# Optimization experiments

Measured on AMD Instinct MI355X. Metric: run time of the kernel, lower is better.

The kernel has to match this reference:

```python
import jax, jax.numpy as jnp
import numpy as np

B, N, D, P_IN, P_OUT = 8, 2048, 32, 8, 4


def setup_inputs() -> dict:
    key = jax.random.key(0)
    k1, k2, k3, k4 = jax.random.split(key, 4)
    U = jax.random.normal(k1, (B, N, D, P_IN), dtype=jnp.float32)
    A = jax.random.uniform(k2, (B, N, N), dtype=jnp.float32)
    W_self = jax.random.normal(k3, (P_IN, P_OUT), dtype=jnp.float32) * 0.01
    W_neigh = jax.random.normal(k4, (P_IN, P_OUT), dtype=jnp.float32) * 0.01
    bias = jnp.zeros((1, 1, 1, P_OUT), dtype=jnp.float32)
    return {"U": U, "A": A, "W_self": W_self, "W_neigh": W_neigh, "bias": bias}


def _stiefel_projection(Y_flat):
    # Polar factor: Y = W S V^T  ->  proj = W V^T (same as Y @ (Y^T Y)^{-1/2})
    u, _, vt = jnp.linalg.svd(Y_flat, full_matrices=False)
    return u @ vt


def reference(U, A, W_self, W_neigh, bias):
    # U: (B,N,d,p_in); A: (B,N,N)
    M_self = jnp.einsum('bndi,io->bndo', U, W_self)
    M_neigh = jnp.einsum('bndi,io->bndo', U, W_neigh)
    # dense neighborhood aggregation: A @ reshape(M_neigh, (B,N,d*p_out))
    M_agg = jnp.einsum('bnm,bmdo->bndo', A, M_neigh)
    Y = jax.nn.relu(M_self + M_agg + bias)
    Y_flat = Y.reshape(B * N, D, P_OUT)
    U_proj = _stiefel_projection(Y_flat)
    return U_proj.reshape(B, N, D, P_OUT)
```

## Files before the change

kernel.cpp:

```cpp
#include <hip/hip_runtime.h>
#include <math.h>

constexpr int B_   = 8;
constexpr int N_   = 2048;
constexpr int D_   = 32;
constexpr int PIN  = 8;
constexpr int POUT = 4;
constexpr int COLS = 128;
constexpr int BM   = 64;
constexpr int BK   = 64;
constexpr int NT   = N_ / BK;

using f32x4  = __attribute__((ext_vector_type(4))) float;
using bf16x8 = __attribute__((ext_vector_type(8))) short;

__device__ __forceinline__ unsigned short f2bf(float f) {
    union { float f; unsigned u; } v; v.f = f;
    unsigned u = v.u + 0x7fffu + ((v.u >> 16) & 1u);
    return (unsigned short)(u >> 16);
}

__global__ __launch_bounds__(256) void mneigh_t_kernel(
    const float* __restrict__ U, const float* __restrict__ Wn,
    unsigned short* __restrict__ Btg)
{
    const int bt = blockIdx.x;
    const int b  = bt >> 5;
    const int n0 = (bt & 31) * 64;
    const int t  = threadIdx.x;
    const int d  = t >> 3;
    const int ns = t & 7;

    float w[PIN][POUT];
#pragma unroll
    for (int p = 0; p < PIN; ++p)
#pragma unroll
        for (int o = 0; o < POUT; ++o) w[p][o] = Wn[p * POUT + o];

    union { unsigned short s[8]; int4 v; } ob[POUT];
    const float* Ub = U + (((size_t)(b * N_ + n0 + ns * 8)) * D_ + d) * PIN;
#pragma unroll
    for (int ni = 0; ni < 8; ++ni) {
        const float4 u0 = *(const float4*)(Ub + (size_t)ni * D_ * PIN);
        const float4 u1 = *(const float4*)(Ub + (size_t)ni * D_ * PIN + 4);
        const float uu[8] = {u0.x, u0.y, u0.z, u0.w, u1.x, u1.y, u1.z, u1.w};
#pragma unroll
        for (int o = 0; o < POUT; ++o) {
            float s = 0.f;
#pragma unroll
            for (int p = 0; p < PIN; ++p) s = fmaf(uu[p], w[p][o], s);
            ob[o].s[ni] = f2bf(s);
        }
    }
#pragma unroll
    for (int o = 0; o < POUT; ++o) {
        unsigned short* dst =
            Btg + ((size_t)(b * COLS + d * 4 + o)) * N_ + n0 + ns * 8;
        *(int4*)dst = ob[o].v;
    }
}

__global__ __launch_bounds__(512) void gemm_proj_kernel(
    const float* __restrict__ A, const unsigned short* __restrict__ Btg,
    const float* __restrict__ U, const float* __restrict__ Wsg,
    const float* __restrict__ bias, float* __restrict__ out)
{
    __shared__ unsigned char smem[49664];
    float* Yl = (float*)smem;
    float* Gp = (float*)(smem + 33792);
    float* Sm = (float*)(smem + 44032);

    const int bid = blockIdx.x;
    const int b   = bid >> 5;
    const int r0  = (bid & 31) * BM;
    const int t   = threadIdx.x;
    const int lane = t & 63, wv = t >> 6;
    const int wr = wv >> 1, wc = wv & 1;
    const int q = lane >> 4, rl = lane & 15;
    const unsigned swz = (unsigned)((lane & 7) << 4);
    const int rA = wr * 16 + rl;

    const int arow = t >> 3, akk = (t & 7) * 8;
    const unsigned aswz = (unsigned)((arow & 7) << 4);
    const int bcol = t >> 2, bk16 = (t & 3) * 16;
    const unsigned bswz = (unsigned)((bcol & 7) << 4);

    const float* Ab = A + (size_t)b * N_ * N_ + (size_t)r0 * N_;
    const unsigned short* Bb = Btg + (size_t)b * COLS * N_;

    f32x4 acc[4] = {f32x4{0,0,0,0}, f32x4{0,0,0,0}, f32x4{0,0,0,0}, f32x4{0,0,0,0}};

    {
        const float4 a0 = *(const float4*)(Ab + (size_t)arow * N_ + akk);
        const float4 a1 = *(const float4*)(Ab + (size_t)arow * N_ + akk + 4);
        const int4 b0 = *(const int4*)(Bb + (size_t)bcol * N_ + bk16);
        const int4 b1 = *(const int4*)(Bb + (size_t)bcol * N_ + bk16 + 8);
        union { unsigned short s[8]; int4 v; } pk;
        pk.s[0] = f2bf(a0.x); pk.s[1] = f2bf(a0.y); pk.s[2] = f2bf(a0.z);
        pk.s[3] = f2bf(a0.w); pk.s[4] = f2bf(a1.x); pk.s[5] = f2bf(a1.y);
        pk.s[6] = f2bf(a1.z); pk.s[7] = f2bf(a1.w);
        *(int4*)(smem + arow * 128 + ((unsigned)(akk * 2) ^ aswz)) = pk.v;
        *(int4*)(smem + 8192 + bcol * 128 + ((unsigned)(bk16 * 2) ^ bswz)) = b0;
        *(int4*)(smem + 8192 + bcol * 128 + ((unsigned)(bk16 * 2 + 16) ^ bswz)) = b1;
    }
    __syncthreads();

    for (int kt = 0; kt < NT; ++kt) {
        float4 na0, na1; int4 nb0, nb1;
        const bool more = (kt + 1 < NT);
        if (more) {
            const int k0 = (kt + 1) * BK;
            na0 = *(const float4*)(Ab + (size_t)arow * N_ + k0 + akk);
            na1 = *(const float4*)(Ab + (size_t)arow * N_ + k0 + akk + 4);
            nb0 = *(const int4*)(Bb + (size_t)bcol * N_ + k0 + bk16);
            nb1 = *(const int4*)(Bb + (size_t)bcol * N_ + k0 + bk16 + 8);
        }
#pragma unroll
        for (int ks = 0; ks < 2; ++ks) {
            const bf16x8 af =
                *(const bf16x8*)(smem + rA * 128 + ((unsigned)(ks * 64 + q * 16) ^ swz));
#pragma unroll
            for (int cf = 0; cf < 4; ++cf) {
                const int rB = wc * 64 + cf * 16 + rl;
                const bf16x8 bfr = *(const bf16x8*)(
                    smem + 8192 + rB * 128 + ((unsigned)(ks * 64 + q * 16) ^ swz));
                acc[cf] = __builtin_amdgcn_mfma_f32_16x16x32_bf16(af, bfr, acc[cf],
                                                                  0, 0, 0);
            }
        }
        __syncthreads();
        if (more) {
            union { unsigned short s[8]; int4 v; } pk;
            pk.s[0] = f2bf(na0.x); pk.s[1] = f2bf(na0.y); pk.s[2] = f2bf(na0.z);
            pk.s[3] = f2bf(na0.w); pk.s[4] = f2bf(na1.x); pk.s[5] = f2bf(na1.y);
            pk.s[6] = f2bf(na1.z); pk.s[7] = f2bf(na1.w);
            *(int4*)(smem + arow * 128 + ((unsigned)(akk * 2) ^ aswz)) = pk.v;
            *(int4*)(smem + 8192 + bcol * 128 + ((unsigned)(bk16 * 2) ^ bswz)) = nb0;
            *(int4*)(smem + 8192 + bcol * 128 + ((unsigned)(bk16 * 2 + 16) ^ bswz)) = nb1;
        }
        __syncthreads();
    }

#pragma unroll
    for (int cf = 0; cf < 4; ++cf)
#pragma unroll
        for (int r = 0; r < 4; ++r) {
            const int row = wr * 16 + q * 4 + r;
            const int col = wc * 64 + cf * 16 + rl;
            Yl[row * 132 + col] = acc[cf][r];
        }
    __syncthreads();

    float ws[PIN][POUT];
#pragma unroll
    for (int p = 0; p < PIN; ++p)
#pragma unroll
        for (int o = 0; o < POUT; ++o) ws[p][o] = Wsg[p * POUT + o];
    const float bz[4] = {bias[0], bias[1], bias[2], bias[3]};
#pragma unroll
    for (int i = 0; i < 4; ++i) {
        const int cell = t + i * 512;
        const int row = cell >> 5, d = cell & 31;
        const float* up = U + (((size_t)(b * N_ + r0 + row)) * D_ + d) * PIN;
        const float4 u0 = *(const float4*)up;
        const float4 u1 = *(const float4*)(up + 4);
        const float uu[8] = {u0.x, u0.y, u0.z, u0.w, u1.x, u1.y, u1.z, u1.w};
#pragma unroll
        for (int o = 0; o < POUT; ++o) {
            float s = bz[o];
#pragma unroll
            for (int p = 0; p < PIN; ++p) s = fmaf(uu[p], ws[p][o], s);
            const int idx = row * 132 + d * 4 + o;
            Yl[idx] = fmaxf(Yl[idx] + s, 0.f);
        }
    }
    __syncthreads();

    if (t < 256) {
        const int row = t >> 2, qd = t & 3;
        float g[10] = {0,0,0,0,0,0,0,0,0,0};
#pragma unroll
        for (int d = qd * 8; d < qd * 8 + 8; ++d) {
            const float4 y = *(const float4*)(Yl + row * 132 + 4 * d);
            g[0] = fmaf(y.x, y.x, g[0]); g[1] = fmaf(y.x, y.y, g[1]);
            g[2] = fmaf(y.x, y.z, g[2]); g[3] = fmaf(y.x, y.w, g[3]);
            g[4] = fmaf(y.y, y.y, g[4]); g[5] = fmaf(y.y, y.z, g[5]);
            g[6] = fmaf(y.y, y.w, g[6]); g[7] = fmaf(y.z, y.z, g[7]);
            g[8] = fmaf(y.z, y.w, g[8]); g[9] = fmaf(y.w, y.w, g[9]);
        }
        float* gp = Gp + (row * 4 + qd) * 10;
#pragma unroll
        for (int k = 0; k < 10; ++k) gp[k] = g[k];
    }
    __syncthreads();

    if (t < 64) {
        float gg[10];
#pragma unroll
        for (int k = 0; k < 10; ++k)
            gg[k] = Gp[(t * 4 + 0) * 10 + k] + Gp[(t * 4 + 1) * 10 + k] +
                    Gp[(t * 4 + 2) * 10 + k] + Gp[(t * 4 + 3) * 10 + k];
        float m[4][4] = {{gg[0], gg[1], gg[2], gg[3]},
                         {gg[1], gg[4], gg[5], gg[6]},
                         {gg[2], gg[5], gg[7], gg[8]},
                         {gg[3], gg[6], gg[8], gg[9]}};
        float v[4][4] = {{1,0,0,0},{0,1,0,0},{0,0,1,0},{0,0,0,1}};
        for (int sweep = 0; sweep < 6; ++sweep) {
#pragma unroll
            for (int p = 0; p < 3; ++p) {
#pragma unroll
                for (int qq = p + 1; qq < 4; ++qq) {
                    const float apq = m[p][qq];
                    if (fabsf(apq) < 1e-28f) continue;
                    const float theta = (m[qq][qq] - m[p][p]) / (2.f * apq);
                    const float tt = copysignf(1.f, theta) /
                        (fabsf(theta) + sqrtf(fmaf(theta, theta, 1.f)));
                    const float c = 1.f / sqrtf(fmaf(tt, tt, 1.f));
                    const float s = tt * c;
#pragma unroll
                    for (int k = 0; k < 4; ++k) {
                        const float mkp = m[k][p], mkq = m[k][qq];
                        m[k][p] = c * mkp - s * mkq;
                        m[k][qq] = s * mkp + c * mkq;
                    }
#pragma unroll
                    for (int k = 0; k < 4; ++k) {
                        const float mpk = m[p][k], mqk = m[qq][k];
                        m[p][k] = c * mpk - s * mqk;
                        m[qq][k] = s * mpk + c * mqk;
                    }
#pragma unroll
                    for (int k = 0; k < 4; ++k) {
                        const float vkp = v[k][p], vkq = v[k][qq];
                        v[k][p] = c * vkp - s * vkq;
                        v[k][qq] = s * vkp + c * vkq;
                    }
                }
            }
        }
        const float lam[4] = {m[0][0], m[1][1], m[2][2], m[3][3]};
        const float lmax = fmaxf(fmaxf(lam[0], lam[1]), fmaxf(lam[2], lam[3]));
        const float lfloor = fmaxf(lmax * 1e-12f, 1e-30f);
        float rlv[4];
#pragma unroll
        for (int k = 0; k < 4; ++k) rlv[k] = 1.f / sqrtf(fmaxf(lam[k], lfloor));
#pragma unroll
        for (int i = 0; i < 4; ++i)
#pragma unroll
            for (int j = 0; j < 4; ++j)
                Sm[t * 16 + i * 4 + j] =
                    v[i][0] * v[j][0] * rlv[0] + v[i][1] * v[j][1] * rlv[1] +
                    v[i][2] * v[j][2] * rlv[2] + v[i][3] * v[j][3] * rlv[3];
    }
    __syncthreads();

#pragma unroll
    for (int i = 0; i < 4; ++i) {
        const int cell = t + i * 512;
        const int row = cell >> 5, d = cell & 31;
        const float4 y = *(const float4*)(Yl + row * 132 + 4 * d);
        const float* S = Sm + row * 16;
        float4 o4;
        o4.x = y.x * S[0]  + y.y * S[4]  + y.z * S[8]  + y.w * S[12];
        o4.y = y.x * S[1]  + y.y * S[5]  + y.z * S[9]  + y.w * S[13];
        o4.z = y.x * S[2]  + y.y * S[6]  + y.z * S[10] + y.w * S[14];
        o4.w = y.x * S[3]  + y.y * S[7]  + y.z * S[11] + y.w * S[15];
        *(float4*)(out + ((size_t)(b * N_ + r0 + row)) * COLS + 4 * d) = o4;
    }
}

extern "C" void kernel_launch(void* const* d_in, const int* in_sizes, int n_in,
                              void* d_out, int out_size, void* d_ws, size_t ws_size,
                              hipStream_t stream)
{
    const float* U      = (const float*)d_in[0];
    const float* A      = (const float*)d_in[1];
    const float* Wself  = (const float*)d_in[2];
    const float* Wneigh = (const float*)d_in[3];
    const float* bias   = (const float*)d_in[4];
    float* out = (float*)d_out;

    unsigned short* Btg = (unsigned short*)d_ws;

    mneigh_t_kernel<<<B_ * (N_ / 64), 256, 0, stream>>>(U, Wneigh, Btg);
    gemm_proj_kernel<<<B_ * (N_ / BM), 512, 0, stream>>>(A, Btg, U, Wself, bias,
                                                         out);
}
```

Measured before the change: 52.57 us.

## Halve row tile, double-buffer LDS, swizzle block order, raise MFMA priority

Shrinks the GEMM row tile from 64 to 32 rows, which doubles the block count to 512 and remaps the 8 waves into a 2x4 grid, each computing two 16x16 fragments. The LDS A/B tiles become double-buffered, so each iteration writes the next tile into the other buffer and needs one barrier instead of two. Block indices are interleaved across batches, and s_setprio raises wave priority around the MFMA section. The aim is more parallelism across CUs and fewer barriers, at the cost of re-reading the shared B operand twice as often.

```diff
diff --git a/kernel.cpp b/kernel.cpp
--- a/kernel.cpp
+++ b/kernel.cpp
@@ -7,7 +7,7 @@
 constexpr int PIN  = 8;
 constexpr int POUT = 4;
 constexpr int COLS = 128;
-constexpr int BM   = 64;
+constexpr int BM   = 32;
 constexpr int BK   = 64;
 constexpr int NT   = N_ / BK;
 
@@ -65,88 +65,92 @@
     const float* __restrict__ U, const float* __restrict__ Wsg,
     const float* __restrict__ bias, float* __restrict__ out)
 {
-    __shared__ unsigned char smem[49664];
+    __shared__ unsigned char smem[40960];
     float* Yl = (float*)smem;
-    float* Gp = (float*)(smem + 33792);
-    float* Sm = (float*)(smem + 44032);
-
-    const int bid = blockIdx.x;
-    const int b   = bid >> 5;
-    const int r0  = (bid & 31) * BM;
+    float* Gp = (float*)(smem + 16896);
+    float* Sm = (float*)(smem + 22016);
+
+    const int bid = (blockIdx.x & 7) * 64 + (blockIdx.x >> 3);
+    const int b   = bid >> 6;
+    const int r0  = (bid & 63) * BM;
     const int t   = threadIdx.x;
     const int lane = t & 63, wv = t >> 6;
-    const int wr = wv >> 1, wc = wv & 1;
+    const int wr = wv >> 2, wc = wv & 3;
     const int q = lane >> 4, rl = lane & 15;
     const unsigned swz = (unsigned)((lane & 7) << 4);
     const int rA = wr * 16 + rl;
 
-    const int arow = t >> 3, akk = (t & 7) * 8;
+    const int arow = t >> 4, af4 = t & 15;
     const unsigned aswz = (unsigned)((arow & 7) << 4);
-    const int bcol = t >> 2, bk16 = (t & 3) * 16;
+    const int bcol = t >> 2, bsg = t & 3;
     const unsigned bswz = (unsigned)((bcol & 7) << 4);
 
     const float* Ab = A + (size_t)b * N_ * N_ + (size_t)r0 * N_;
     const unsigned short* Bb = Btg + (size_t)b * COLS * N_;
 
-    f32x4 acc[4] = {f32x4{0,0,0,0}, f32x4{0,0,0,0}, f32x4{0,0,0,0}, f32x4{0,0,0,0}};
+    f32x4 acc[2] = {f32x4{0, 0, 0, 0}, f32x4{0, 0, 0, 0}};
 
     {
-        const float4 a0 = *(const float4*)(Ab + (size_t)arow * N_ + akk);
-        const float4 a1 = *(const float4*)(Ab + (size_t)arow * N_ + akk + 4);
-        const int4 b0 = *(const int4*)(Bb + (size_t)bcol * N_ + bk16);
-        const int4 b1 = *(const int4*)(Bb + (size_t)bcol * N_ + bk16 + 8);
-        union { unsigned short s[8]; int4 v; } pk;
-        pk.s[0] = f2bf(a0.x); pk.s[1] = f2bf(a0.y); pk.s[2] = f2bf(a0.z);
-        pk.s[3] = f2bf(a0.w); pk.s[4] = f2bf(a1.x); pk.s[5] = f2bf(a1.y);
-        pk.s[6] = f2bf(a1.z); pk.s[7] = f2bf(a1.w);
-        *(int4*)(smem + arow * 128 + ((unsigned)(akk * 2) ^ aswz)) = pk.v;
-        *(int4*)(smem + 8192 + bcol * 128 + ((unsigned)(bk16 * 2) ^ bswz)) = b0;
-        *(int4*)(smem + 8192 + bcol * 128 + ((unsigned)(bk16 * 2 + 16) ^ bswz)) = b1;
+        const float4 a0 = *(const float4*)(Ab + (size_t)arow * N_ + af4 * 4);
+        const int4 b0 = *(const int4*)(Bb + (size_t)bcol * N_ + bsg * 16);
+        const int4 b1 = *(const int4*)(Bb + (size_t)bcol * N_ + bsg * 16 + 8);
+        union { unsigned short s[4]; int2 v; } pk;
+        pk.s[0] = f2bf(a0.x); pk.s[1] = f2bf(a0.y);
+        pk.s[2] = f2bf(a0.z); pk.s[3] = f2bf(a0.w);
+        *(int2*)(smem + arow * 128 + ((unsigned)(af4 * 8) ^ aswz)) = pk.v;
+        *(int4*)(smem + 8192 + bcol * 128 + ((unsigned)(bsg * 32) ^ bswz)) = b0;
+        *(int4*)(smem + 8192 + bcol * 128 + ((unsigned)(bsg * 32 + 16) ^ bswz)) = b1;
     }
     __syncthreads();
 
     for (int kt = 0; kt < NT; ++kt) {
-        float4 na0, na1; int4 nb0, nb1;
+        const unsigned cur = (unsigned)(kt & 1);
+        const unsigned nxt = cur ^ 1u;
+        float4 na0; int4 nb0, nb1;
         const bool more = (kt + 1 < NT);
         if (more) {
             const int k0 = (kt + 1) * BK;
-            na0 = *(const float4*)(Ab + (size_t)arow * N_ + k0 + akk);
-            na1 = *(const float4*)(Ab + (size_t)arow * N_ + k0 + akk + 4);
-            nb0 = *(const int4*)(Bb + (size_t)bcol * N_ + k0 + bk16);
-            nb1 = *(const int4*)(Bb + (size_t)bcol * N_ + k0 + bk16 + 8);
-        }
+            na0 = *(const float4*)(Ab + (size_t)arow * N_ + k0 + af4 * 4);
+            nb0 = *(const int4*)(Bb + (size_t)bcol * N_ + k0 + bsg * 16);
+            nb1 = *(const int4*)(Bb + (size_t)bcol * N_ + k0 + bsg * 16 + 8);
+        }
+        const unsigned abase = cur * 4096u;
+        const unsigned bbase = 8192u + cur * 16384u;
+        __builtin_amdgcn_s_setprio(1);
 #pragma unroll
         for (int ks = 0; ks < 2; ++ks) {
-            const bf16x8 af =
-                *(const bf16x8*)(smem + rA * 128 + ((unsigned)(ks * 64 + q * 16) ^ swz));
-#pragma unroll
-            for (int cf = 0; cf < 4; ++cf) {
-                const int rB = wc * 64 + cf * 16 + rl;
+            const bf16x8 af = *(const bf16x8*)(
+                smem + abase + rA * 128 + ((unsigned)(ks * 64 + q * 16) ^ swz));
+#pragma unroll
+            for (int cf = 0; cf < 2; ++cf) {
+                const int rB = wc * 32 + cf * 16 + rl;
                 const bf16x8 bfr = *(const bf16x8*)(
-                    smem + 8192 + rB * 128 + ((unsigned)(ks * 64 + q * 16) ^ swz));
+                    smem + bbase + rB * 128 + ((unsigned)(ks * 64 + q * 16) ^ swz));
                 acc[cf] = __builtin_amdgcn_mfma_f32_16x16x32_bf16(af, bfr, acc[cf],
                                                                   0, 0, 0);
             }
         }
+        __builtin_amdgcn_s_setprio(0);
+        if (more) {
+            union { unsigned short s[4]; int2 v; } pk;
+            pk.s[0] = f2bf(na0.x); pk.s[1] = f2bf(na0.y);
+            pk.s[2] = f2bf(na0.z); pk.s[3] = f2bf(na0.w);
+            *(int2*)(smem + nxt * 4096u + arow * 128 +
+                     ((unsigned)(af4 * 8) ^ aswz)) = pk.v;
+            *(int4*)(smem + 8192u + nxt * 16384u + bcol * 128 +
+                     ((unsigned)(bsg * 32) ^ bswz)) = nb0;
+            *(int4*)(smem + 8192u + nxt * 16384u + bcol * 128 +
+                     ((unsigned)(bsg * 32 + 16) ^ bswz)) = nb1;
+        }
         __syncthreads();
-        if (more) {
-            union { unsigned short s[8]; int4 v; } pk;
-            pk.s[0] = f2bf(na0.x); pk.s[1] = f2bf(na0.y); pk.s[2] = f2bf(na0.z);
-            pk.s[3] = f2bf(na0.w); pk.s[4] = f2bf(na1.x); pk.s[5] = f2bf(na1.y);
-            pk.s[6] = f2bf(na1.z); pk.s[7] = f2bf(na1.w);
-            *(int4*)(smem + arow * 128 + ((unsigned)(akk * 2) ^ aswz)) = pk.v;
-            *(int4*)(smem + 8192 + bcol * 128 + ((unsigned)(bk16 * 2) ^ bswz)) = nb0;
-            *(int4*)(smem + 8192 + bcol * 128 + ((unsigned)(bk16 * 2 + 16) ^ bswz)) = nb1;
-        }
-        __syncthreads();
-    }
-
-#pragma unroll
-    for (int cf = 0; cf < 4; ++cf)
+    }
+
+#pragma unroll
+    for (int cf = 0; cf < 2; ++cf)
 #pragma unroll
         for (int r = 0; r < 4; ++r) {
             const int row = wr * 16 + q * 4 + r;
-            const int col = wc * 64 + cf * 16 + rl;
+            const int col = wc * 32 + cf * 16 + rl;
             Yl[row * 132 + col] = acc[cf][r];
         }
     __syncthreads();
@@ -158,7 +162,7 @@
         for (int o = 0; o < POUT; ++o) ws[p][o] = Wsg[p * POUT + o];
     const float bz[4] = {bias[0], bias[1], bias[2], bias[3]};
 #pragma unroll
-    for (int i = 0; i < 4; ++i) {
+    for (int i = 0; i < 2; ++i) {
         const int cell = t + i * 512;
         const int row = cell >> 5, d = cell & 31;
         const float* up = U + (((size_t)(b * N_ + r0 + row)) * D_ + d) * PIN;
@@ -176,7 +180,7 @@
     }
     __syncthreads();
 
-    if (t < 256) {
+    if (t < 128) {
         const int row = t >> 2, qd = t & 3;
         float g[10] = {0,0,0,0,0,0,0,0,0,0};
 #pragma unroll
@@ -194,7 +198,7 @@
     }
     __syncthreads();
 
-    if (t < 64) {
+    if (t < 32) {
         float gg[10];
 #pragma unroll
         for (int k = 0; k < 10; ++k)
@@ -255,7 +259,7 @@
     __syncthreads();
 
 #pragma unroll
-    for (int i = 0; i < 4; ++i) {
+    for (int i = 0; i < 2; ++i) {
         const int cell = t + i * 512;
         const int row = cell >> 5, d = cell & 31;
         const float4 y = *(const float4*)(Yl + row * 132 + 4 * d);
```

Result: faster. 48.60 us, median of 4 (-7.6%).
